# Kernel optimization log

Hardware: AMD Instinct MI355X
Metric: run time of the kernel (lower is better)

## Reference

```python
import jax, jax.numpy as jnp
import numpy as np

N = 100000       # nodes
E = 3200000      # edges
F_IN = 128       # num_node_features
DIM = 32         # hidden dim (fixed in Net1)
L = 3            # num_layers
C = 10           # num_classes


def setup_inputs() -> dict:
    key = jax.random.key(0)
    ks = jax.random.split(key, 16)
    x = jax.random.normal(ks[0], (N, F_IN), dtype=jnp.float32)
    src = jax.random.randint(ks[1], (E,), 0, N, dtype=jnp.int32)
    dst = jax.random.randint(ks[2], (E,), 0, N, dtype=jnp.int32)
    def glorot(k, shape):
        lim = np.sqrt(6.0 / (shape[0] + shape[1])).astype(np.float32)
        return jax.random.uniform(k, shape, jnp.float32, -lim, lim)
    dims = [F_IN, DIM, DIM]
    inp = {"x": x, "src": src, "dst": dst}
    for i in range(L):
        din = dims[i]
        inp[f"Wn{i}"] = glorot(ks[3 + 3 * i], (din, DIM))      # neighbor weight
        inp[f"bn{i}"] = jnp.zeros((DIM,), jnp.float32)          # neighbor bias
        inp[f"Ws{i}"] = glorot(ks[4 + 3 * i], (din, DIM))      # self weight (no bias)
    inp["fc_w"] = glorot(ks[13], (DIM * L + F_IN, C))
    inp["fc_b"] = jnp.zeros((C,), jnp.float32)
    return inp


def _graph_conv_wl(x, src, dst, Wn, bn, Ws):
    # GraphConv(norm='none'): transform then aggregate (sum over in-neighbors)
    h = x @ Wn                                   # [N, DIM]
    msg = h[src]                                 # [E, DIM] gather
    agg = jax.ops.segment_sum(msg, dst, num_segments=N)  # [N, DIM] scatter-add
    return agg + bn + x @ Ws


def reference(x, src, dst, Wn0, bn0, Ws0, Wn1, bn1, Ws1, Wn2, bn2, Ws2, fc_w, fc_b):
    params = [(Wn0, bn0, Ws0), (Wn1, bn1, Ws1), (Wn2, bn2, Ws2)]
    xs = [x]
    h = x
    for Wn, bn, Ws in params:
        h = jax.nn.relu(_graph_conv_wl(h, src, dst, Wn, bn, Ws))
        xs.append(h)
    h = jnp.concatenate(xs, axis=1)              # [N, 128 + 3*32]
    logits = h @ fc_w + fc_b                     # [N, C]
    return jax.nn.log_softmax(logits, axis=1)
```

## Files before the change

kernel.cpp:

```cpp
#include <hip/hip_runtime.h>
#include <cstdint>

#define NN 100000
#define EE 3200000
#define SB_BITS 8
#define SB_NODES (1 << SB_BITS)
#define NSB ((NN + SB_NODES - 1) / SB_NODES)
#define CAP 9216
#define CH 4096
#define EPT (CH / 256)

__device__ inline float4 add4(float4 a, float4 b) {
    return make_float4(a.x + b.x, a.y + b.y, a.z + b.z, a.w + b.w);
}


__global__ void k_hist_sb(const int* __restrict__ dst, int* __restrict__ scnt) {
    __shared__ int h[NSB];
    for (int i = threadIdx.x; i < NSB; i += 256) h[i] = 0;
    __syncthreads();
    for (int e = blockIdx.x * 256 + threadIdx.x; e < EE; e += gridDim.x * 256)
        atomicAdd(&h[dst[e] >> SB_BITS], 1);
    __syncthreads();
    for (int i = threadIdx.x; i < NSB; i += 256) {
        int v = h[i];
        if (v) atomicAdd(&scnt[i], v);
    }
}

__global__ void k_scan_sb(const int* __restrict__ scnt,
                          int* __restrict__ sbptr, int* __restrict__ cursor) {
    __shared__ int sm[512];
    int i = threadIdx.x;
    int v0 = (i < NSB) ? scnt[i] : 0;
    int v1 = (i + 256 < NSB) ? scnt[i + 256] : 0;
    sm[i] = v0;
    sm[i + 256] = v1;
    __syncthreads();
    for (int o = 1; o < 512; o <<= 1) {
        int a0 = (i >= o) ? sm[i - o] : 0;
        int a1 = (i + 256 >= o) ? sm[i + 256 - o] : 0;
        __syncthreads();
        sm[i] += a0;
        sm[i + 256] += a1;
        __syncthreads();
    }
    if (i < NSB)       { sbptr[i]       = sm[i] - v0;       cursor[i]       = sm[i] - v0; }
    if (i + 256 < NSB) { sbptr[i + 256] = sm[i + 256] - v1; cursor[i + 256] = sm[i + 256] - v1; }
    if (i == 0) sbptr[NSB] = sm[511];
}

__global__ void k_split(const int* __restrict__ src, const int* __restrict__ dst,
                        int* __restrict__ cursor, int* __restrict__ out) {
    __shared__ int hist[512];
    __shared__ int lbase[NSB];
    __shared__ int gbase[NSB];
    __shared__ int buf[CH];
    __shared__ unsigned short keyb[CH];
    const int nchunks = (EE + CH - 1) / CH;
    for (int c = blockIdx.x; c < nchunks; c += gridDim.x) {
        int base = c * CH;
        int cnt = min(CH, EE - base);
        hist[threadIdx.x] = 0;
        hist[threadIdx.x + 256] = 0;
        __syncthreads();
        int words[EPT], ranks[EPT], keys[EPT];
        #pragma unroll
        for (int k = 0; k < EPT; ++k) {
            int idx = threadIdx.x + k * 256;
            if (idx < cnt) {
                int d = dst[base + idx];
                int s = src[base + idx];
                int key = d >> SB_BITS;
                words[k] = s | ((d & (SB_NODES - 1)) << 17);
                keys[k] = key;
                ranks[k] = atomicAdd(&hist[key], 1);
            } else keys[k] = -1;
        }
        __syncthreads();
        int i = threadIdx.x;
        int v0 = hist[i], v1 = hist[i + 256];
        for (int o = 1; o < 512; o <<= 1) {
            int a0 = (i >= o) ? hist[i - o] : 0;
            int a1 = (i + 256 >= o) ? hist[i + 256 - o] : 0;
            __syncthreads();
            hist[i] += a0;
            hist[i + 256] += a1;
            __syncthreads();
        }
        if (i < NSB) {
            lbase[i] = hist[i] - v0;
            gbase[i] = (v0 > 0) ? atomicAdd(&cursor[i], v0) : 0;
        }
        if (i + 256 < NSB) {
            lbase[i + 256] = hist[i + 256] - v1;
            gbase[i + 256] = (v1 > 0) ? atomicAdd(&cursor[i + 256], v1) : 0;
        }
        __syncthreads();
        #pragma unroll
        for (int k = 0; k < EPT; ++k) {
            if (keys[k] >= 0) {
                int p = lbase[keys[k]] + ranks[k];
                buf[p] = words[k];
                keyb[p] = (unsigned short)keys[k];
            }
        }
        __syncthreads();
        for (int j = threadIdx.x; j < cnt; j += 256) {
            int kk = keyb[j];
            out[gbase[kk] + (j - lbase[kk])] = buf[j];
        }
        __syncthreads();
    }
}

__global__ void k_sb_sort(const int* __restrict__ sbptr, const int* __restrict__ packed,
                          int* __restrict__ csr_src, int* __restrict__ rowptr) {
    __shared__ int hist[SB_NODES];
    __shared__ int lbuf[CAP];
    int b = blockIdx.x;
    int e0 = sbptr[b], e1 = sbptr[b + 1];
    int cnt = e1 - e0;
    hist[threadIdx.x] = 0;
    __syncthreads();
    for (int j = e0 + threadIdx.x; j < e1; j += 256)
        atomicAdd(&hist[(packed[j] >> 17) & (SB_NODES - 1)], 1);
    __syncthreads();
    int i = threadIdx.x;
    int v = hist[i];
    for (int o = 1; o < 256; o <<= 1) {
        int a = (i >= o) ? hist[i - o] : 0;
        __syncthreads();
        hist[i] += a;
        __syncthreads();
    }
    int excl = hist[i] - v;
    int node = (b << SB_BITS) + i;
    if (node < NN) rowptr[node] = e0 + excl;
    hist[i] = excl;
    if (b == 0 && i == 0) rowptr[NN] = EE;
    __syncthreads();
    if (cnt <= CAP) {
        for (int j = e0 + threadIdx.x; j < e1; j += 256) {
            int w = packed[j];
            int n = (w >> 17) & (SB_NODES - 1);
            int pos = atomicAdd(&hist[n], 1);
            lbuf[pos] = w & 0x1FFFF;
        }
        __syncthreads();
        for (int j = threadIdx.x; j < cnt; j += 256)
            csr_src[e0 + j] = lbuf[j];
    } else {
        for (int j = e0 + threadIdx.x; j < e1; j += 256) {
            int w = packed[j];
            int n = (w >> 17) & (SB_NODES - 1);
            int pos = atomicAdd(&hist[n], 1);
            csr_src[e0 + pos] = w & 0x1FFFF;
        }
    }
}


template <int DIN>
__global__ __launch_bounds__(256) void k_transform(
        const float* __restrict__ h,
        const float* __restrict__ Wn,
        const float* __restrict__ Ws,
        const float* __restrict__ bn,
        float* __restrict__ t,
        float* __restrict__ hout) {
    constexpr int KC = 16;
    __shared__ float hs[256 * (KC + 1)];
    const int which = blockIdx.x & 1;
    const int node = (blockIdx.x >> 1) * 256 + threadIdx.x;
    const bool valid = node < NN;
    const float* __restrict__ W = which ? Ws : Wn;
    const float* __restrict__ hr = h + (size_t)(valid ? node : NN - 1) * DIN;
    float acc[32];
    #pragma unroll
    for (int d = 0; d < 32; ++d) acc[d] = 0.f;
    for (int kc = 0; kc < DIN; kc += KC) {
        __syncthreads();
        #pragma unroll
        for (int j = 0; j < KC / 4; ++j) {
            float4 f = *(const float4*)(hr + kc + j * 4);
            hs[threadIdx.x * (KC + 1) + j * 4 + 0] = f.x;
            hs[threadIdx.x * (KC + 1) + j * 4 + 1] = f.y;
            hs[threadIdx.x * (KC + 1) + j * 4 + 2] = f.z;
            hs[threadIdx.x * (KC + 1) + j * 4 + 3] = f.w;
        }
        __syncthreads();
        #pragma unroll
        for (int kk = 0; kk < KC; ++kk) {
            float f = hs[threadIdx.x * (KC + 1) + kk];
            const float* __restrict__ w0 = W + (kc + kk) * 32;
            #pragma unroll
            for (int d = 0; d < 32; ++d) acc[d] = fmaf(f, w0[d], acc[d]);
        }
    }
    if (valid) {
        if (which) {
            #pragma unroll
            for (int d = 0; d < 32; ++d) acc[d] += bn[d];
        }
        float* __restrict__ dstp = (which ? hout : t) + (size_t)node * 32;
        #pragma unroll
        for (int d = 0; d < 32; d += 4)
            *(float4*)(dstp + d) = make_float4(acc[d], acc[d + 1], acc[d + 2], acc[d + 3]);
    }
}

__global__ void k_aggregate(const int* __restrict__ rowptr,
                            const int* __restrict__ csr_src,
                            const float4* __restrict__ t4,
                            float4* __restrict__ hout4) {
    int node = blockIdx.x * 32 + (threadIdx.x >> 3);
    int q = threadIdx.x & 7;
    if (node >= NN) return;
    int j = rowptr[node];
    int end = rowptr[node + 1];
    float4 a0 = make_float4(0.f, 0.f, 0.f, 0.f);
    float4 a1 = a0, a2 = a0, a3 = a0;
    for (; j + 4 <= end; j += 4) {
        int s0 = csr_src[j];
        int s1 = csr_src[j + 1];
        int s2 = csr_src[j + 2];
        int s3 = csr_src[j + 3];
        a0 = add4(a0, t4[s0 * 8 + q]);
        a1 = add4(a1, t4[s1 * 8 + q]);
        a2 = add4(a2, t4[s2 * 8 + q]);
        a3 = add4(a3, t4[s3 * 8 + q]);
    }
    for (; j < end; ++j) a0 = add4(a0, t4[csr_src[j] * 8 + q]);
    float4 s = add4(add4(a0, a1), add4(a2, a3));
    int idx = node * 8 + q;
    float4 h = hout4[idx];
    h.x = fmaxf(h.x + s.x, 0.f);
    h.y = fmaxf(h.y + s.y, 0.f);
    h.z = fmaxf(h.z + s.z, 0.f);
    h.w = fmaxf(h.w + s.w, 0.f);
    hout4[idx] = h;
}

__global__ void k_final(const float* __restrict__ x,
                        const float* __restrict__ h1,
                        const float* __restrict__ h2,
                        const float* __restrict__ h3,
                        const float* __restrict__ fc_w,
                        const float* __restrict__ fc_b,
                        float* __restrict__ out) {
    __shared__ float Wl[224 * 10];
    __shared__ float bl[10];
    for (int i = threadIdx.x; i < 224 * 10; i += blockDim.x) Wl[i] = fc_w[i];
    if (threadIdx.x < 10) bl[threadIdx.x] = fc_b[threadIdx.x];
    __syncthreads();
    int n = blockIdx.x * blockDim.x + threadIdx.x;
    if (n >= NN) return;
    float acc[10];
    #pragma unroll
    for (int c = 0; c < 10; ++c) acc[c] = bl[c];
    const float* xr = x + (size_t)n * 128;
    for (int j = 0; j < 128; ++j) {
        float f = xr[j];
        #pragma unroll
        for (int c = 0; c < 10; ++c) acc[c] += f * Wl[j * 10 + c];
    }
    const float* hs[3] = {h1, h2, h3};
    for (int l = 0; l < 3; ++l) {
        const float* hr = hs[l] + (size_t)n * 32;
        for (int j = 0; j < 32; ++j) {
            float f = hr[j];
            #pragma unroll
            for (int c = 0; c < 10; ++c) acc[c] += f * Wl[(128 + l * 32 + j) * 10 + c];
        }
    }
    float m = acc[0];
    #pragma unroll
    for (int c = 1; c < 10; ++c) m = fmaxf(m, acc[c]);
    float s = 0.f;
    #pragma unroll
    for (int c = 0; c < 10; ++c) s += __expf(acc[c] - m);
    float ls = __logf(s);
    #pragma unroll
    for (int c = 0; c < 10; ++c) out[n * 10 + c] = acc[c] - m - ls;
}

extern "C" void kernel_launch(void* const* d_in, const int* in_sizes, int n_in,
                              void* d_out, int out_size, void* d_ws, size_t ws_size,
                              hipStream_t stream) {
    const float* x   = (const float*)d_in[0];
    const int*   src = (const int*)d_in[1];
    const int*   dst = (const int*)d_in[2];
    const float* Wn[3] = {(const float*)d_in[3], (const float*)d_in[6], (const float*)d_in[9]};
    const float* bn[3] = {(const float*)d_in[4], (const float*)d_in[7], (const float*)d_in[10]};
    const float* Ws[3] = {(const float*)d_in[5], (const float*)d_in[8], (const float*)d_in[11]};
    const float* fc_w = (const float*)d_in[12];
    const float* fc_b = (const float*)d_in[13];
    float* out = (float*)d_out;

    char* w = (char*)d_ws;
    const size_t NF = (size_t)NN * 32;
    float* t   = (float*)w;                     w += NF * 4;
    float* h1  = (float*)w;                     w += NF * 4;
    float* h2  = (float*)w;                     w += NF * 4;
    float* h3  = (float*)w;                     w += NF * 4;
    int* csr_src = (int*)w;                     w += (size_t)EE * 4;
    int* scnt   = (int*)w;                      w += (size_t)NSB * 4;
    int* sbptr  = (int*)w;                      w += (size_t)(NSB + 1) * 4;
    int* cursor = (int*)w;                      w += (size_t)NSB * 4;
    int* rowptr = (int*)w;                      w += (size_t)(NN + 1) * 4;
    int* packed = (int*)h3;
    float* hbuf[3] = {h1, h2, h3};

    hipMemsetAsync(scnt, 0, (size_t)NSB * 4, stream);
    k_hist_sb<<<512, 256, 0, stream>>>(dst, scnt);
    k_scan_sb<<<1, 256, 0, stream>>>(scnt, sbptr, cursor);
    k_split<<<512, 256, 0, stream>>>(src, dst, cursor, packed);
    k_sb_sort<<<NSB, 256, 0, stream>>>(sbptr, packed, csr_src, rowptr);

    const int tr_blocks = 2 * ((NN + 255) / 256);
    const int ag_blocks = (NN + 31) / 32;
    k_transform<128><<<tr_blocks, 256, 0, stream>>>(x, Wn[0], Ws[0], bn[0], t, h1);
    k_aggregate<<<ag_blocks, 256, 0, stream>>>(rowptr, csr_src, (const float4*)t, (float4*)h1);
    k_transform<32><<<tr_blocks, 256, 0, stream>>>(h1, Wn[1], Ws[1], bn[1], t, h2);
    k_aggregate<<<ag_blocks, 256, 0, stream>>>(rowptr, csr_src, (const float4*)t, (float4*)h2);
    k_transform<32><<<tr_blocks, 256, 0, stream>>>(h2, Wn[2], Ws[2], bn[2], t, h3);
    k_aggregate<<<ag_blocks, 256, 0, stream>>>(rowptr, csr_src, (const float4*)t, (float4*)h3);
    k_final<<<(NN + 255) / 256, 256, 0, stream>>>(x, h1, h2, h3, fc_w, fc_b, out);
}
```

Baseline: 472.9 us.

## Store neighbor transform in bf16 and fuse both weight products per block

After: 536.4 us. +13.4%, slower.

```diff
diff --git a/kernel.cpp b/kernel.cpp
--- a/kernel.cpp
+++ b/kernel.cpp
@@ -12,6 +12,14 @@
 
 __device__ inline float4 add4(float4 a, float4 b) {
     return make_float4(a.x + b.x, a.y + b.y, a.z + b.z, a.w + b.w);
+}
+
+__device__ inline unsigned pk_bf2(float lo, float hi) {
+    unsigned a = __float_as_uint(lo);
+    unsigned b = __float_as_uint(hi);
+    a = (a + 0x7FFFu + ((a >> 16) & 1u)) >> 16;
+    b = (b + 0x7FFFu + ((b >> 16) & 1u)) & 0xFFFF0000u;
+    return a | b;
 }
 
 
@@ -167,52 +175,63 @@
         const float* __restrict__ Wn,
         const float* __restrict__ Ws,
         const float* __restrict__ bn,
-        float* __restrict__ t,
+        unsigned* __restrict__ t_bf,
         float* __restrict__ hout) {
     constexpr int KC = 16;
+    constexpr int V4 = KC / 4;
     __shared__ float hs[256 * (KC + 1)];
-    const int which = blockIdx.x & 1;
-    const int node = (blockIdx.x >> 1) * 256 + threadIdx.x;
+    const int node0 = blockIdx.x * 256;
+    const int node = node0 + threadIdx.x;
     const bool valid = node < NN;
-    const float* __restrict__ W = which ? Ws : Wn;
-    const float* __restrict__ hr = h + (size_t)(valid ? node : NN - 1) * DIN;
-    float acc[32];
-    #pragma unroll
-    for (int d = 0; d < 32; ++d) acc[d] = 0.f;
+    float an[32], as[32];
+    #pragma unroll
+    for (int d = 0; d < 32; ++d) { an[d] = 0.f; as[d] = 0.f; }
     for (int kc = 0; kc < DIN; kc += KC) {
         __syncthreads();
         #pragma unroll
-        for (int j = 0; j < KC / 4; ++j) {
-            float4 f = *(const float4*)(hr + kc + j * 4);
-            hs[threadIdx.x * (KC + 1) + j * 4 + 0] = f.x;
-            hs[threadIdx.x * (KC + 1) + j * 4 + 1] = f.y;
-            hs[threadIdx.x * (KC + 1) + j * 4 + 2] = f.z;
-            hs[threadIdx.x * (KC + 1) + j * 4 + 3] = f.w;
+        for (int it = 0; it < V4; ++it) {
+            int idx = threadIdx.x + it * 256;
+            int row = idx >> 2;
+            int col = (idx & 3) * 4;
+            int rnode = node0 + row;
+            const float* p = h + (size_t)(rnode < NN ? rnode : NN - 1) * DIN + kc + col;
+            float4 f = *(const float4*)p;
+            hs[row * (KC + 1) + col + 0] = f.x;
+            hs[row * (KC + 1) + col + 1] = f.y;
+            hs[row * (KC + 1) + col + 2] = f.z;
+            hs[row * (KC + 1) + col + 3] = f.w;
         }
         __syncthreads();
         #pragma unroll
         for (int kk = 0; kk < KC; ++kk) {
             float f = hs[threadIdx.x * (KC + 1) + kk];
-            const float* __restrict__ w0 = W + (kc + kk) * 32;
+            const float* __restrict__ w0 = Wn + (kc + kk) * 32;
+            const float* __restrict__ w1 = Ws + (kc + kk) * 32;
             #pragma unroll
-            for (int d = 0; d < 32; ++d) acc[d] = fmaf(f, w0[d], acc[d]);
+            for (int d = 0; d < 32; ++d) an[d] = fmaf(f, w0[d], an[d]);
+            #pragma unroll
+            for (int d = 0; d < 32; ++d) as[d] = fmaf(f, w1[d], as[d]);
         }
     }
     if (valid) {
-        if (which) {
-            #pragma unroll
-            for (int d = 0; d < 32; ++d) acc[d] += bn[d];
-        }
-        float* __restrict__ dstp = (which ? hout : t) + (size_t)node * 32;
+        unsigned tb[16];
+        #pragma unroll
+        for (int d = 0; d < 16; ++d) tb[d] = pk_bf2(an[2 * d], an[2 * d + 1]);
+        unsigned* tp = t_bf + (size_t)node * 16;
+        #pragma unroll
+        for (int d = 0; d < 16; d += 4)
+            *(uint4*)(tp + d) = make_uint4(tb[d], tb[d + 1], tb[d + 2], tb[d + 3]);
+        float* __restrict__ hp = hout + (size_t)node * 32;
         #pragma unroll
         for (int d = 0; d < 32; d += 4)
-            *(float4*)(dstp + d) = make_float4(acc[d], acc[d + 1], acc[d + 2], acc[d + 3]);
+            *(float4*)(hp + d) = make_float4(as[d] + bn[d], as[d + 1] + bn[d + 1],
+                                             as[d + 2] + bn[d + 2], as[d + 3] + bn[d + 3]);
     }
 }
 
 __global__ void k_aggregate(const int* __restrict__ rowptr,
                             const int* __restrict__ csr_src,
-                            const float4* __restrict__ t4,
+                            const uint2* __restrict__ t2,
                             float4* __restrict__ hout4) {
     int node = blockIdx.x * 32 + (threadIdx.x >> 3);
     int q = threadIdx.x & 7;
@@ -226,12 +245,24 @@
         int s1 = csr_src[j + 1];
         int s2 = csr_src[j + 2];
         int s3 = csr_src[j + 3];
-        a0 = add4(a0, t4[s0 * 8 + q]);
-        a1 = add4(a1, t4[s1 * 8 + q]);
-        a2 = add4(a2, t4[s2 * 8 + q]);
-        a3 = add4(a3, t4[s3 * 8 + q]);
-    }
-    for (; j < end; ++j) a0 = add4(a0, t4[csr_src[j] * 8 + q]);
+        uint2 u0 = t2[s0 * 8 + q];
+        uint2 u1 = t2[s1 * 8 + q];
+        uint2 u2 = t2[s2 * 8 + q];
+        uint2 u3 = t2[s3 * 8 + q];
+        a0.x += __uint_as_float(u0.x << 16); a0.y += __uint_as_float(u0.x & 0xFFFF0000u);
+        a0.z += __uint_as_float(u0.y << 16); a0.w += __uint_as_float(u0.y & 0xFFFF0000u);
+        a1.x += __uint_as_float(u1.x << 16); a1.y += __uint_as_float(u1.x & 0xFFFF0000u);
+        a1.z += __uint_as_float(u1.y << 16); a1.w += __uint_as_float(u1.y & 0xFFFF0000u);
+        a2.x += __uint_as_float(u2.x << 16); a2.y += __uint_as_float(u2.x & 0xFFFF0000u);
+        a2.z += __uint_as_float(u2.y << 16); a2.w += __uint_as_float(u2.y & 0xFFFF0000u);
+        a3.x += __uint_as_float(u3.x << 16); a3.y += __uint_as_float(u3.x & 0xFFFF0000u);
+        a3.z += __uint_as_float(u3.y << 16); a3.w += __uint_as_float(u3.y & 0xFFFF0000u);
+    }
+    for (; j < end; ++j) {
+        uint2 u = t2[csr_src[j] * 8 + q];
+        a0.x += __uint_as_float(u.x << 16); a0.y += __uint_as_float(u.x & 0xFFFF0000u);
+        a0.z += __uint_as_float(u.y << 16); a0.w += __uint_as_float(u.y & 0xFFFF0000u);
+    }
     float4 s = add4(add4(a0, a1), add4(a2, a3));
     int idx = node * 8 + q;
     float4 h = hout4[idx];
@@ -300,7 +331,7 @@
 
     char* w = (char*)d_ws;
     const size_t NF = (size_t)NN * 32;
-    float* t   = (float*)w;                     w += NF * 4;
+    unsigned* t_bf = (unsigned*)w;              w += (size_t)NN * 16 * 4;
     float* h1  = (float*)w;                     w += NF * 4;
     float* h2  = (float*)w;                     w += NF * 4;
     float* h3  = (float*)w;                     w += NF * 4;
@@ -310,7 +341,6 @@
     int* cursor = (int*)w;                      w += (size_t)NSB * 4;
     int* rowptr = (int*)w;                      w += (size_t)(NN + 1) * 4;
     int* packed = (int*)h3;
-    float* hbuf[3] = {h1, h2, h3};
 
     hipMemsetAsync(scnt, 0, (size_t)NSB * 4, stream);
     k_hist_sb<<<512, 256, 0, stream>>>(dst, scnt);
@@ -318,13 +348,13 @@
     k_split<<<512, 256, 0, stream>>>(src, dst, cursor, packed);
     k_sb_sort<<<NSB, 256, 0, stream>>>(sbptr, packed, csr_src, rowptr);
 
-    const int tr_blocks = 2 * ((NN + 255) / 256);
+    const int tr_blocks = (NN + 255) / 256;
     const int ag_blocks = (NN + 31) / 32;
-    k_transform<128><<<tr_blocks, 256, 0, stream>>>(x, Wn[0], Ws[0], bn[0], t, h1);
-    k_aggregate<<<ag_blocks, 256, 0, stream>>>(rowptr, csr_src, (const float4*)t, (float4*)h1);
-    k_transform<32><<<tr_blocks, 256, 0, stream>>>(h1, Wn[1], Ws[1], bn[1], t, h2);
-    k_aggregate<<<ag_blocks, 256, 0, stream>>>(rowptr, csr_src, (const float4*)t, (float4*)h2);
-    k_transform<32><<<tr_blocks, 256, 0, stream>>>(h2, Wn[2], Ws[2], bn[2], t, h3);
-    k_aggregate<<<ag_blocks, 256, 0, stream>>>(rowptr, csr_src, (const float4*)t, (float4*)h3);
+    k_transform<128><<<tr_blocks, 256, 0, stream>>>(x, Wn[0], Ws[0], bn[0], t_bf, h1);
+    k_aggregate<<<ag_blocks, 256, 0, stream>>>(rowptr, csr_src, (const uint2*)t_bf, (float4*)h1);
+    k_transform<32><<<tr_blocks, 256, 0, stream>>>(h1, Wn[1], Ws[1], bn[1], t_bf, h2);
+    k_aggregate<<<ag_blocks, 256, 0, stream>>>(rowptr, csr_src, (const uint2*)t_bf, (float4*)h2);
+    k_transform<32><<<tr_blocks, 256, 0, stream>>>(h2, Wn[2], Ws[2], bn[2], t_bf, h3);
+    k_aggregate<<<ag_blocks, 256, 0, stream>>>(rowptr, csr_src, (const uint2*)t_bf, (float4*)h3);
     k_final<<<(NN + 255) / 256, 256, 0, stream>>>(x, h1, h2, h3, fc_w, fc_b, out);
 }
```
